# Performance work log

Measured on AMD Instinct MI355X. Metric: run time of the kernel, lower is better.

Reference implementation:

```python
import jax, jax.numpy as jnp
import numpy as np

N_NODES = 10000
N_EDGES = 160000
D_IN = 128
D_EMB = 512
D_HID = 256
GAT_SLOPE = 0.2   # PyG GATv2Conv default negative_slope
MLP_SLOPE = 0.1   # relu_alpha


def _glorot(key, shape):
    fan_in, fan_out = shape[0], shape[-1]
    lim = np.sqrt(6.0 / (fan_in + fan_out))
    return jax.random.uniform(key, shape, jnp.float32, -lim, lim)


def setup_inputs() -> dict:
    key = jax.random.key(0)
    ks = jax.random.split(key, 20)
    inp = {
        'x': jax.random.normal(ks[0], (N_NODES, D_IN), jnp.float32),
        'edge_index': jax.random.randint(ks[1], (2, N_EDGES), 0, N_NODES, jnp.int64),
    }
    # GATv2 layers: (Wl, Wr, att, bias) each
    dims = [(D_IN, D_EMB), (D_EMB, D_EMB), (D_EMB, D_EMB)]
    for i, (di, do) in enumerate(dims, start=1):
        inp[f'Wl{i}'] = _glorot(ks[2 + 4 * i], (di, do))
        inp[f'Wr{i}'] = _glorot(ks[3 + 4 * i], (di, do))
        inp[f'att{i}'] = _glorot(ks[4 + 4 * i], (1, do))[0]
        inp[f'b{i}'] = jnp.zeros((do,), jnp.float32)
    # MLP
    inp['A1'] = _glorot(ks[2], (D_EMB, D_HID)); inp['c1'] = jnp.zeros((D_HID,), jnp.float32)
    inp['A2'] = _glorot(ks[3], (D_HID, D_HID)); inp['c2'] = jnp.zeros((D_HID,), jnp.float32)
    inp['A3'] = _glorot(ks[4], (D_HID, 1));     inp['c3'] = jnp.zeros((1,), jnp.float32)
    return inp


def gatv2_conv(x, src, dst, Wl, Wr, att, bias):
    # PyG GATv2Conv, heads=1: xl = source transform, xr = target transform
    xl = x @ Wl                                   # [N, D]
    xr = x @ Wr                                   # [N, D]
    # per-edge attention logit: att . leaky_relu(xl[src] + xr[dst])
    e = jax.nn.leaky_relu(xl[src] + xr[dst], GAT_SLOPE) @ att   # [E]
    # segment softmax over incoming edges of each dst node
    emax = jax.ops.segment_max(e, dst, num_segments=N_NODES)    # [N]
    w = jnp.exp(e - emax[dst])
    denom = jax.ops.segment_sum(w, dst, num_segments=N_NODES)   # [N]
    alpha = w / (denom[dst] + 1e-16)                             # [E]
    out = jax.ops.segment_sum(alpha[:, None] * xl[src], dst, num_segments=N_NODES)
    return out + bias


def reference(x, edge_index, Wl1, Wr1, att1, b1, Wl2, Wr2, att2, b2,
              Wl3, Wr3, att3, b3, A1, c1, A2, c2, A3, c3):
    src, dst = edge_index[0], edge_index[1]
    h = jnp.tanh(gatv2_conv(x, src, dst, Wl1, Wr1, att1, b1))
    h = jnp.tanh(gatv2_conv(h, src, dst, Wl2, Wr2, att2, b2))
    h = jnp.tanh(gatv2_conv(h, src, dst, Wl3, Wr3, att3, b3))
    h = jax.nn.leaky_relu(h @ A1 + c1, MLP_SLOPE)
    h = jax.nn.leaky_relu(h @ A2 + c2, MLP_SLOPE)
    logits = h @ A3 + c3                          # [N, 1]
    return jax.nn.softmax(logits, axis=0)         # softmax over nodes
```

## Files before the change

### kernel.cpp

```cpp
#include <hip/hip_runtime.h>
#include <hip/hip_bf16.h>

#define N_NODES 10000
#define N_EDGES 160000
#define D_IN    128
#define D_EMB   512
#define D_HID   256
#define DMAX    512

typedef unsigned short u16;
typedef __attribute__((ext_vector_type(8))) short short8;
typedef __attribute__((ext_vector_type(4))) float floatx4;

__device__ __forceinline__ float bf2f(u16 u) {
    union { unsigned int i; float f; } v; v.i = ((unsigned int)u) << 16; return v.f;
}
__device__ __forceinline__ u16 f2bf(float f) {
    union { float f; unsigned int i; } v; v.f = f;
    unsigned int x = v.i;
    return (u16)((x + 0x7fffu + ((x >> 16) & 1u)) >> 16);
}
__device__ __forceinline__ float inval(const void* p, int fp32, int idx) {
    return fp32 ? ((const float*)p)[idx] : bf2f(((const u16*)p)[idx]);
}

__device__ __forceinline__ void gld_lds16(const u16* g, u16* l) {
    __builtin_amdgcn_global_load_lds((const __attribute__((address_space(1))) void*)g,
                                     (__attribute__((address_space(3))) void*)l,
                                     16, 0, 0);
}

__device__ __forceinline__ int edge_src(const int* __restrict__ ei, int flg, int e) {
    int v = flg ? ei[2 * e] : ei[e];
    return min(max(v, 0), N_NODES - 1);
}
__device__ __forceinline__ int edge_dst(const int* __restrict__ ei, int flg, int e) {
    int v = flg ? ei[2 * N_EDGES + 2 * e] : ei[N_EDGES + e];
    return min(max(v, 0), N_NODES - 1);
}

__global__ void sentinel_kernel(float* out, int n) {
    int i = blockIdx.x * 256 + threadIdx.x;
    if (i < n) out[i] = 1.0f;
}

__global__ __launch_bounds__(256)
void detect_zero_kernel(const int* __restrict__ ei, const u16* __restrict__ xu,
                        int* flag, int* counts, float* logits) {
    int gid = blockIdx.x * 256 + threadIdx.x;
    for (int i = gid; i < N_NODES; i += gridDim.x * 256) { counts[i] = 0; logits[i] = 0.f; }
    if (blockIdx.x != 0) return;
    __shared__ int s_or[256];
    __shared__ int s_cnt[256];
    int t = threadIdx.x;
    int v = 0;
    for (int k = t; k < 4096; k += 256) v |= ei[1 + 2 * k];
    int c = 0;
    for (int k = t; k < 4096; k += 256) {
        u16 u = xu[k];
        int ex = (u >> 7) & 0xFF;
        bool plaus = (u == 0) || (ex >= 64 && ex <= 191);
        if (!plaus) c++;
    }
    s_or[t] = v; s_cnt[t] = c;
    __syncthreads();
    for (int off = 128; off > 0; off >>= 1) {
        if (t < off) { s_or[t] |= s_or[t + off]; s_cnt[t] += s_cnt[t + off]; }
        __syncthreads();
    }
    if (t == 0) {
        flag[0] = (s_or[0] == 0) ? 1 : 0;
        flag[1] = (s_cnt[0] > 256) ? 1 : 0;
    }
}

struct ConvJobs {
    const void* src[10];
    u16* dh[10];
    u16* dl[10];
    int rows[10], cols[10], trans[10];
    int cum[11];
    int njobs;
};

__global__ __launch_bounds__(256)
void convert_fused_kernel(ConvJobs jobs, const int* __restrict__ flag) {
    int idx = blockIdx.x * 256 + threadIdx.x;
    if (idx >= jobs.cum[jobs.njobs]) return;
    int fp32 = flag[1];
    int jb = 0;
    while (idx >= jobs.cum[jb + 1]) jb++;
    int local = idx - jobs.cum[jb];
    float v = inval(jobs.src[jb], fp32, local);
    u16 hi = f2bf(v);
    int o;
    if (jobs.trans[jb]) {
        int r = local / jobs.cols[jb], c = local % jobs.cols[jb];
        o = c * jobs.rows[jb] + r;
    } else o = local;
    jobs.dh[jb][o] = hi;
    if (jobs.dl[jb]) jobs.dl[jb][o] = f2bf(v - bf2f(hi));
}

__global__ void count_edges_kernel(const int* __restrict__ ei, const int* __restrict__ flag,
                                   int* counts) {
    int e = blockIdx.x * 256 + threadIdx.x;
    if (e < N_EDGES) atomicAdd(&counts[edge_dst(ei, flag[0], e)], 1);
}

__global__ __launch_bounds__(256)
void scan_counts_kernel(int* counts, int* rowptr) {
    __shared__ int part[256];
    int tid = threadIdx.x;
    const int CH = 40;
    int base = tid * CH;
    int loc[CH];
    int s = 0;
    #pragma unroll
    for (int i = 0; i < CH; i++) {
        int idx = base + i;
        int c = (idx < N_NODES) ? counts[idx] : 0;
        loc[i] = s; s += c;
    }
    part[tid] = s;
    __syncthreads();
    for (int off = 1; off < 256; off <<= 1) {
        int v = part[tid];
        int add = (tid >= off) ? part[tid - off] : 0;
        __syncthreads();
        part[tid] = v + add;
        __syncthreads();
    }
    int pre = (tid > 0) ? part[tid - 1] : 0;
    #pragma unroll
    for (int i = 0; i < CH; i++) {
        int idx = base + i;
        if (idx < N_NODES) { int v = pre + loc[i]; rowptr[idx] = v; counts[idx] = v; }
    }
    if (tid == 255) rowptr[N_NODES] = part[255];
}

__global__ void fill_esrcp_kernel(const int* __restrict__ ei, const int* __restrict__ flag,
                                  int* counts, int* esrcp) {
    int e = blockIdx.x * 256 + threadIdx.x;
    if (e < N_EDGES) {
        int flg = flag[0];
        int pos = atomicAdd(&counts[edge_dst(ei, flg, e)], 1);
        if (pos >= 0 && pos < N_EDGES) esrcp[pos] = edge_src(ei, flg, e);
    }
}

__global__ __launch_bounds__(256)
void lpt_order_kernel(const int* __restrict__ rowptr, int* __restrict__ order) {
    __shared__ int hist[DMAX];
    __shared__ int off[DMAX];
    __shared__ int part[256];
    int t = threadIdx.x;
    for (int d = t; d < DMAX; d += 256) hist[d] = 0;
    __syncthreads();
    for (int n = t; n < N_NODES; n += 256) {
        int d = min(rowptr[n + 1] - rowptr[n], DMAX - 1);
        atomicAdd(&hist[d], 1);
    }
    __syncthreads();
    int d0 = (DMAX - 1) - 2 * t;
    int d1 = d0 - 1;
    int c0 = hist[d0], c1 = hist[d1];
    part[t] = c0 + c1;
    __syncthreads();
    for (int o = 1; o < 256; o <<= 1) {
        int v = part[t];
        int add = (t >= o) ? part[t - o] : 0;
        __syncthreads();
        part[t] = v + add;
        __syncthreads();
    }
    int pre = (t > 0) ? part[t - 1] : 0;
    off[d0] = pre;
    off[d1] = pre + c0;
    __syncthreads();
    for (int n = t; n < N_NODES; n += 256) {
        int d = min(rowptr[n + 1] - rowptr[n], DMAX - 1);
        int pos = atomicAdd(&off[d], 1);
        if (pos >= 0 && pos < N_NODES) order[pos] = n;
    }
}

__global__ __launch_bounds__(256)
void gemm_dual_kernel(const u16* __restrict__ Ah, const u16* __restrict__ Al,
                      const u16* __restrict__ B0h, const u16* __restrict__ B1h,
                      u16* __restrict__ C0, float* __restrict__ C1,
                      int M, int N, int K)
{
    __shared__ u16 sAh[128 * 32];
    __shared__ u16 sAl[128 * 32];
    __shared__ u16 sBh[128 * 32];
    int nb = N >> 7;
    int half = (int)blockIdx.x >= nb;
    int bx = half ? (blockIdx.x - nb) : blockIdx.x;
    const u16* BTh = half ? B1h : B0h;

    int tid = threadIdx.x;
    int lane = tid & 63, wv = tid >> 6;
    int l15 = lane & 15, l4 = lane >> 4;
    int wr = (wv >> 1) * 64, wc = (wv & 1) * 64;
    int m0 = blockIdx.y * 128, n0 = bx * 128;

    int i0 = tid, i1 = tid + 256;
    int r0 = i0 >> 2, b0 = i0 & 3, sb0 = b0 ^ ((r0 >> 1) & 3);
    int r1 = i1 >> 2, b1 = i1 & 3, sb1 = b1 ^ ((r1 >> 1) & 3);
    int gr0 = min(m0 + r0, M - 1), gr1 = min(m0 + r1, M - 1);
    const u16* a0p = Ah + (size_t)gr0 * K + sb0 * 8;
    const u16* a1p = Ah + (size_t)gr1 * K + sb1 * 8;
    const u16* l0p = Al + (size_t)gr0 * K + sb0 * 8;
    const u16* l1p = Al + (size_t)gr1 * K + sb1 * 8;
    const u16* bb0p = BTh + (size_t)(n0 + r0) * K + sb0 * 8;
    const u16* bb1p = BTh + (size_t)(n0 + r1) * K + sb1 * 8;
    u16* lA0 = &sAh[(size_t)(wv * 64) * 8];
    u16* lA1 = &sAh[(size_t)(256 + wv * 64) * 8];
    u16* lL0 = &sAl[(size_t)(wv * 64) * 8];
    u16* lL1 = &sAl[(size_t)(256 + wv * 64) * 8];
    u16* lB0 = &sBh[(size_t)(wv * 64) * 8];
    u16* lB1 = &sBh[(size_t)(256 + wv * 64) * 8];

    floatx4 acc[4][4];
    #pragma unroll
    for (int i = 0; i < 4; i++)
        #pragma unroll
        for (int j = 0; j < 4; j++) acc[i][j] = (floatx4){0.f, 0.f, 0.f, 0.f};

    int aoff[4], boff[4];
    #pragma unroll
    for (int i = 0; i < 4; i++) {
        int arow = wr + i * 16 + l15;
        aoff[i] = arow * 32 + ((l4 ^ ((arow >> 1) & 3)) << 3);
        int bcol = wc + i * 16 + l15;
        boff[i] = bcol * 32 + ((l4 ^ ((bcol >> 1) & 3)) << 3);
    }

    for (int kk = 0; kk < K; kk += 32) {
        __syncthreads();
        gld_lds16(a0p + kk, lA0);
        gld_lds16(a1p + kk, lA1);
        gld_lds16(l0p + kk, lL0);
        gld_lds16(l1p + kk, lL1);
        gld_lds16(bb0p + kk, lB0);
        gld_lds16(bb1p + kk, lB1);
        __syncthreads();

        short8 ah[4], al[4];
        #pragma unroll
        for (int i = 0; i < 4; i++) {
            ah[i] = *(const short8*)(&sAh[aoff[i]]);
            al[i] = *(const short8*)(&sAl[aoff[i]]);
        }
        #pragma unroll
        for (int j = 0; j < 4; j++) {
            short8 bh = *(const short8*)(&sBh[boff[j]]);
            #pragma unroll
            for (int i = 0; i < 4; i++) {
                acc[i][j] = __builtin_amdgcn_mfma_f32_16x16x32_bf16(ah[i], bh, acc[i][j], 0, 0, 0);
                acc[i][j] = __builtin_amdgcn_mfma_f32_16x16x32_bf16(al[i], bh, acc[i][j], 0, 0, 0);
            }
        }
    }

    #pragma unroll
    for (int j = 0; j < 4; j++) {
        int col = n0 + wc + j * 16 + l15;
        #pragma unroll
        for (int i = 0; i < 4; i++) {
            #pragma unroll
            for (int r = 0; r < 4; r++) {
                int row = m0 + wr + i * 16 + l4 * 4 + r;
                if (row < M) {
                    if (half) C1[(size_t)row * N + col] = acc[i][j][r];
                    else      C0[(size_t)row * N + col] = f2bf(acc[i][j][r]);
                }
            }
        }
    }
}

template<int FUSE>
__global__ __launch_bounds__(256)
void gemm_mlp64_kernel(const u16* __restrict__ Ah, const u16* __restrict__ Al,
                       const u16* __restrict__ BTh,
                       u16* __restrict__ Ch, u16* __restrict__ Cl,
                       const void* __restrict__ biasraw,
                       const void* __restrict__ A3raw, float* __restrict__ logits,
                       const int* __restrict__ flag,
                       int M, int N, int K)
{
    __shared__ u16 sAh[64 * 32];
    __shared__ u16 sAl[64 * 32];
    __shared__ u16 sBh[64 * 32];
    int tid = threadIdx.x;
    int lane = tid & 63, wv = tid >> 6;
    int l15 = lane & 15, l4 = lane >> 4;
    int m0 = blockIdx.y * 64, n0 = blockIdx.x * 64;

    int r = (tid >> 2), blk = tid & 3, sb = blk ^ ((r >> 1) & 3);
    int gr = min(m0 + r, M - 1);
    const u16* ap = Ah + (size_t)gr * K + sb * 8;
    const u16* lp = Al + (size_t)gr * K + sb * 8;
    const u16* bp = BTh + (size_t)(n0 + r) * K + sb * 8;
    u16* lA = &sAh[(size_t)(wv * 64) * 8];
    u16* lL = &sAl[(size_t)(wv * 64) * 8];
    u16* lB = &sBh[(size_t)(wv * 64) * 8];

    floatx4 acc[4];
    #pragma unroll
    for (int j = 0; j < 4; j++) acc[j] = (floatx4){0.f, 0.f, 0.f, 0.f};

    int arow = wv * 16 + l15;
    int aoff = arow * 32 + ((l4 ^ ((arow >> 1) & 3)) << 3);
    int boff[4];
    #pragma unroll
    for (int j = 0; j < 4; j++) {
        int bcol = j * 16 + l15;
        boff[j] = bcol * 32 + ((l4 ^ ((bcol >> 1) & 3)) << 3);
    }

    for (int kk = 0; kk < K; kk += 32) {
        __syncthreads();
        gld_lds16(ap + kk, lA);
        gld_lds16(lp + kk, lL);
        gld_lds16(bp + kk, lB);
        __syncthreads();

        short8 ah = *(const short8*)(&sAh[aoff]);
        short8 al = *(const short8*)(&sAl[aoff]);
        #pragma unroll
        for (int j = 0; j < 4; j++) {
            short8 bh = *(const short8*)(&sBh[boff[j]]);
            acc[j] = __builtin_amdgcn_mfma_f32_16x16x32_bf16(ah, bh, acc[j], 0, 0, 0);
            acc[j] = __builtin_amdgcn_mfma_f32_16x16x32_bf16(al, bh, acc[j], 0, 0, 0);
        }
    }

    const int fp32 = flag[1];
    float lsum[4] = {0.f, 0.f, 0.f, 0.f};
    #pragma unroll
    for (int j = 0; j < 4; j++) {
        int col = n0 + j * 16 + l15;
        float bv = inval(biasraw, fp32, col);
        float a3 = FUSE ? inval(A3raw, fp32, col) : 0.f;
        #pragma unroll
        for (int rr = 0; rr < 4; rr++) {
            int row = m0 + wv * 16 + l4 * 4 + rr;
            if (row < M) {
                float v = acc[j][rr] + bv;
                v = v > 0.f ? v : 0.1f * v;
                if (FUSE) {
                    lsum[rr] += v * a3;
                } else {
                    u16 hi = f2bf(v);
                    Ch[(size_t)row * N + col] = hi;
                    Cl[(size_t)row * N + col] = f2bf(v - bf2f(hi));
                }
            }
        }
    }
    if (FUSE) {
        #pragma unroll
        for (int rr = 0; rr < 4; rr++) {
            float s = lsum[rr];
            s += __shfl_xor(s, 1);
            s += __shfl_xor(s, 2);
            s += __shfl_xor(s, 4);
            s += __shfl_xor(s, 8);
            int row = m0 + wv * 16 + l4 * 4 + rr;
            if (l15 == 0 && row < M) atomicAdd(&logits[row], s);
        }
    }
}

__global__ __launch_bounds__(256)
void gat_wave_kernel(const int* __restrict__ rowptr, const int* __restrict__ esrcp,
                     const int* __restrict__ order,
                     const u16* __restrict__ xlb, const float* __restrict__ xr,
                     const void* __restrict__ att, const void* __restrict__ bias,
                     const int* __restrict__ flag,
                     u16* __restrict__ hh, u16* __restrict__ hl)
{
    int lane = threadIdx.x & 63, wv = threadIdx.x >> 6;
    int slot = blockIdx.x * 4 + wv;
    if (slot >= N_NODES) return;
    int n = order[slot];
    n = min(max(n, 0), N_NODES - 1);
    int fp32 = flag[1];
    int d0 = lane * 8;
    int l3 = lane & 3;

    int beg = rowptr[n], end = rowptr[n + 1];
    int deg = end - beg;
    int ng = (deg + 3) >> 2;

    const u16* xbase = xlb + d0;

    const float* xrr = xr + (size_t)n * D_EMB;
    float4 r0 = *(const float4*)(xrr + d0);
    float4 r1 = *(const float4*)(xrr + d0 + 4);
    float xrv[8] = {r0.x, r0.y, r0.z, r0.w, r1.x, r1.y, r1.z, r1.w};
    float attv[8];
    #pragma unroll
    for (int k = 0; k < 8; k++) attv[k] = inval(att, fp32, d0 + k);

    float m_run = -3.4e38f, s_run = 0.f;
    float acc[8] = {0.f, 0.f, 0.f, 0.f, 0.f, 0.f, 0.f, 0.f};

    auto ldidx = [&](int g) -> int {
        return esrcp[min(beg + 4 * g + l3, N_EDGES - 1)];
    };

    if (ng > 0) {
        int i0 = ldidx(0);
        uint4 cu0, cu1, cu2, cu3;
        {
            int s0 = __shfl(i0, 0), s1 = __shfl(i0, 1), s2 = __shfl(i0, 2), s3 = __shfl(i0, 3);
            cu0 = *(const uint4*)(xbase + (size_t)s0 * D_EMB);
            cu1 = *(const uint4*)(xbase + (size_t)s1 * D_EMB);
            cu2 = *(const uint4*)(xbase + (size_t)s2 * D_EMB);
            cu3 = *(const uint4*)(xbase + (size_t)s3 * D_EMB);
        }
        int nidx = (ng > 1) ? ldidx(1) : 0;

        for (int g = 0; g < ng; g++) {
            uint4 nu0, nu1, nu2, nu3;
            int nidx2 = 0;
            bool have_next = (g + 1 < ng);
            if (have_next) {
                int t0 = __shfl(nidx, 0), t1 = __shfl(nidx, 1),
                    t2 = __shfl(nidx, 2), t3 = __shfl(nidx, 3);
                nu0 = *(const uint4*)(xbase + (size_t)t0 * D_EMB);
                nu1 = *(const uint4*)(xbase + (size_t)t1 * D_EMB);
                nu2 = *(const uint4*)(xbase + (size_t)t2 * D_EMB);
                nu3 = *(const uint4*)(xbase + (size_t)t3 * D_EMB);
                if (g + 2 < ng) nidx2 = ldidx(g + 2);
            }

            union { uint4 q; u16 us[8]; } u0, u1, u2, u3;
            u0.q = cu0; u1.q = cu1; u2.q = cu2; u3.q = cu3;
            float v0[8], v1[8], v2[8], v3[8];
            #pragma unroll
            for (int k = 0; k < 8; k++) {
                v0[k] = bf2f(u0.us[k]); v1[k] = bf2f(u1.us[k]);
                v2[k] = bf2f(u2.us[k]); v3[k] = bf2f(u3.us[k]);
            }
            float e0 = 0.f, e1 = 0.f, e2 = 0.f, e3 = 0.f;
            #pragma unroll
            for (int k = 0; k < 8; k++) {
                float t0 = v0[k] + xrv[k]; t0 = fmaxf(t0, 0.2f * t0); e0 += attv[k] * t0;
                float t1 = v1[k] + xrv[k]; t1 = fmaxf(t1, 0.2f * t1); e1 += attv[k] * t1;
                float t2 = v2[k] + xrv[k]; t2 = fmaxf(t2, 0.2f * t2); e2 += attv[k] * t2;
                float t3 = v3[k] + xrv[k]; t3 = fmaxf(t3, 0.2f * t3); e3 += attv[k] * t3;
            }
            #pragma unroll
            for (int o = 32; o > 0; o >>= 1) {
                e0 += __shfl_xor(e0, o);
                e1 += __shfl_xor(e1, o);
                e2 += __shfl_xor(e2, o);
                e3 += __shfl_xor(e3, o);
            }
            int base = beg + 4 * g;
            if (base + 1 >= end) e1 = -3.4e38f;
            if (base + 2 >= end) e2 = -3.4e38f;
            if (base + 3 >= end) e3 = -3.4e38f;
            float m4 = fmaxf(fmaxf(e0, e1), fmaxf(e2, e3));
            float m_new = fmaxf(m_run, m4);
            float sc = __expf(m_run - m_new);
            float w0 = __expf(e0 - m_new), w1 = __expf(e1 - m_new);
            float w2 = __expf(e2 - m_new), w3 = __expf(e3 - m_new);
            s_run = s_run * sc + (w0 + w1) + (w2 + w3);
            #pragma unroll
            for (int k = 0; k < 8; k++)
                acc[k] = acc[k] * sc + w0 * v0[k] + w1 * v1[k] + w2 * v2[k] + w3 * v3[k];
            m_run = m_new;

            if (have_next) {
                cu0 = nu0; cu1 = nu1; cu2 = nu2; cu3 = nu3;
                nidx = nidx2;
            }
        }
    }

    float inv = 1.f / (s_run + 1e-16f);
    union { uint4 q; u16 us[8]; } ph, pl;
    #pragma unroll
    for (int k = 0; k < 8; k++) {
        float h = tanhf(acc[k] * inv + inval(bias, fp32, d0 + k));
        u16 hi = f2bf(h);
        ph.us[k] = hi;
        pl.us[k] = f2bf(h - bf2f(hi));
    }
    *(uint4*)(&hh[(size_t)n * D_EMB + d0]) = ph.q;
    *(uint4*)(&hl[(size_t)n * D_EMB + d0]) = pl.q;
}

__global__ __launch_bounds__(256)
void softmax_kernel(const float* __restrict__ logits, float* __restrict__ out)
{
    __shared__ float red[4];
    __shared__ float s_m, s_s;
    int tid = threadIdx.x, lane = tid & 63, wv = tid >> 6;
    float m = -3.4e38f;
    for (int i = tid; i < N_NODES; i += 256) m = fmaxf(m, logits[i]);
    #pragma unroll
    for (int o = 32; o > 0; o >>= 1) m = fmaxf(m, __shfl_down(m, o));
    if (lane == 0) red[wv] = m;
    __syncthreads();
    if (tid == 0) {
        float mm = red[0];
        for (int i = 1; i < 4; i++) mm = fmaxf(mm, red[i]);
        s_m = mm;
    }
    __syncthreads();
    float mm = s_m;
    float s = 0.f;
    for (int i = tid; i < N_NODES; i += 256) s += __expf(logits[i] - mm);
    #pragma unroll
    for (int o = 32; o > 0; o >>= 1) s += __shfl_down(s, o);
    if (lane == 0) red[wv] = s;
    __syncthreads();
    if (tid == 0) {
        float ss = 0.f;
        for (int i = 0; i < 4; i++) ss += red[i];
        s_s = ss;
    }
    __syncthreads();
    float invs = 1.f / s_s;
    for (int i = tid; i < N_NODES; i += 256) out[i] = __expf(logits[i] - mm) * invs;
}

extern "C" void kernel_launch(void* const* d_in, const int* in_sizes, int n_in,
                              void* d_out, int out_size, void* d_ws, size_t ws_size,
                              hipStream_t stream)
{
    const void* x   = d_in[0];
    const int*  ei  = (const int*)d_in[1];
    const void* Wl[3]  = {d_in[2],  d_in[6],  d_in[10]};
    const void* Wr[3]  = {d_in[3],  d_in[7],  d_in[11]};
    const void* att[3] = {d_in[4],  d_in[8],  d_in[12]};
    const void* bia[3] = {d_in[5],  d_in[9],  d_in[13]};
    const void* A1 = d_in[14];
    const void* c1 = d_in[15];
    const void* A2 = d_in[16];
    const void* c2 = d_in[17];
    const void* A3 = d_in[18];

    char* p = (char*)d_ws;
    auto alloc = [&](size_t bytes) {
        char* r = p;
        p += (bytes + 255) & ~(size_t)255;
        return r;
    };
    u16*   xlb    = (u16*)  alloc((size_t)N_NODES * D_EMB * 4);
    float* xr     = (float*)alloc((size_t)N_NODES * D_EMB * 4);
    u16*   hh     = (u16*)  alloc((size_t)N_NODES * D_EMB * 2);
    u16*   hl     = (u16*)  alloc((size_t)N_NODES * D_EMB * 2);
    int*   esrcp  = (int*)  alloc((size_t)N_EDGES * 4);
    int*   rowptr = (int*)  alloc((size_t)(N_NODES + 1) * 4);
    int*   counts = (int*)  alloc((size_t)N_NODES * 4);
    int*   flag   = (int*)  alloc(256);
    float* logits = (float*)alloc((size_t)N_NODES * 4);
    int*   order  = (int*)  alloc((size_t)N_NODES * 4);
    u16* wl1h = (u16*)alloc(D_EMB * D_IN  * 2);
    u16* wr1h = (u16*)alloc(D_EMB * D_IN  * 2);
    u16* wl2h = (u16*)alloc(D_EMB * D_EMB * 2);
    u16* wr2h = (u16*)alloc(D_EMB * D_EMB * 2);
    u16* wl3h = (u16*)alloc(D_EMB * D_EMB * 2);
    u16* wr3h = (u16*)alloc(D_EMB * D_EMB * 2);
    u16* a1h  = (u16*)alloc(D_EMB * D_HID * 2);
    u16* a2h  = (u16*)alloc(D_HID * D_HID * 2);
    u16* xph  = (u16*)alloc((size_t)N_NODES * D_IN * 2);
    u16* xpl  = (u16*)alloc((size_t)N_NODES * D_IN * 2);
    size_t needed = (size_t)(p - (char*)d_ws);

    if (ws_size < needed) {
        sentinel_kernel<<<(out_size + 255) / 256, 256, 0, stream>>>((float*)d_out, out_size);
        return;
    }

    u16* m1h = (u16*)xlb;
    u16* m1l = (u16*)((char*)xlb + 5120000);

    detect_zero_kernel<<<40, 256, 0, stream>>>(ei, (const u16*)x, flag, counts, logits);
    count_edges_kernel<<<(N_EDGES + 255) / 256, 256, 0, stream>>>(ei, flag, counts);
    scan_counts_kernel<<<1, 256, 0, stream>>>(counts, rowptr);
    fill_esrcp_kernel<<<(N_EDGES + 255) / 256, 256, 0, stream>>>(ei, flag, counts, esrcp);

    lpt_order_kernel<<<1, 256, 0, stream>>>(rowptr, order);

    ConvJobs jobs;
    auto setjob = [&](int i, const void* s, u16* dh, u16* dl, int r, int c, int tr) {
        jobs.src[i] = s; jobs.dh[i] = dh; jobs.dl[i] = dl;
        jobs.rows[i] = r; jobs.cols[i] = c; jobs.trans[i] = tr;
    };
    setjob(0, x,     xph,  xpl,     N_NODES, D_IN, 0);
    setjob(1, Wl[0], wl1h, nullptr, D_IN,  D_EMB, 1);
    setjob(2, Wr[0], wr1h, nullptr, D_IN,  D_EMB, 1);
    setjob(3, Wl[1], wl2h, nullptr, D_EMB, D_EMB, 1);
    setjob(4, Wr[1], wr2h, nullptr, D_EMB, D_EMB, 1);
    setjob(5, Wl[2], wl3h, nullptr, D_EMB, D_EMB, 1);
    setjob(6, Wr[2], wr3h, nullptr, D_EMB, D_EMB, 1);
    setjob(7, A1,    a1h,  nullptr, D_EMB, D_HID, 1);
    setjob(8, A2,    a2h,  nullptr, D_HID, D_HID, 1);
    jobs.njobs = 9;
    jobs.cum[0] = 0;
    for (int i = 0; i < 9; i++) jobs.cum[i + 1] = jobs.cum[i] + jobs.rows[i] * jobs.cols[i];
    int ctotal = jobs.cum[9];
    convert_fused_kernel<<<(ctotal + 255) / 256, 256, 0, stream>>>(jobs, flag);

    dim3 gdual(2 * D_EMB / 128, (N_NODES + 127) / 128);
    dim3 gmlp64(D_HID / 64, (N_NODES + 63) / 64);
    int gatgrid = (N_NODES + 3) / 4;

    gemm_dual_kernel<<<gdual, 256, 0, stream>>>(xph, xpl, wl1h, wr1h, xlb, xr, N_NODES, D_EMB, D_IN);
    gat_wave_kernel<<<gatgrid, 256, 0, stream>>>(rowptr, esrcp, order, xlb, xr, att[0], bia[0], flag, hh, hl);
    gemm_dual_kernel<<<gdual, 256, 0, stream>>>(hh, hl, wl2h, wr2h, xlb, xr, N_NODES, D_EMB, D_EMB);
    gat_wave_kernel<<<gatgrid, 256, 0, stream>>>(rowptr, esrcp, order, xlb, xr, att[1], bia[1], flag, hh, hl);
    gemm_dual_kernel<<<gdual, 256, 0, stream>>>(hh, hl, wl3h, wr3h, xlb, xr, N_NODES, D_EMB, D_EMB);
    gat_wave_kernel<<<gatgrid, 256, 0, stream>>>(rowptr, esrcp, order, xlb, xr, att[2], bia[2], flag, hh, hl);

    gemm_mlp64_kernel<0><<<gmlp64, 256, 0, stream>>>(hh, hl, a1h, m1h, m1l, c1, nullptr, nullptr, flag, N_NODES, D_HID, D_EMB);
    gemm_mlp64_kernel<1><<<gmlp64, 256, 0, stream>>>(m1h, m1l, a2h, nullptr, nullptr, c2, A3, logits, flag, N_NODES, D_HID, D_HID);
    softmax_kernel<<<1, 256, 0, stream>>>(logits, (float*)d_out);
}
```

Measured before the change: 438.9 us.

## Parallelize LPT degree-ordering across blocks with histogram, scan, scatter kernels

```diff
diff --git a/kernel.cpp b/kernel.cpp
--- a/kernel.cpp
+++ b/kernel.cpp
@@ -46,9 +46,10 @@
 
 __global__ __launch_bounds__(256)
 void detect_zero_kernel(const int* __restrict__ ei, const u16* __restrict__ xu,
-                        int* flag, int* counts, float* logits) {
+                        int* flag, int* counts, float* logits, int* ghist) {
     int gid = blockIdx.x * 256 + threadIdx.x;
     for (int i = gid; i < N_NODES; i += gridDim.x * 256) { counts[i] = 0; logits[i] = 0.f; }
+    for (int i = gid; i < DMAX; i += gridDim.x * 256) ghist[i] = 0;
     if (blockIdx.x != 0) return;
     __shared__ int s_or[256];
     __shared__ int s_cnt[256];
@@ -151,21 +152,30 @@
 }
 
 __global__ __launch_bounds__(256)
-void lpt_order_kernel(const int* __restrict__ rowptr, int* __restrict__ order) {
-    __shared__ int hist[DMAX];
-    __shared__ int off[DMAX];
+void lpt_hist_kernel(const int* __restrict__ rowptr, int* __restrict__ ghist) {
+    __shared__ int lhist[DMAX];
+    int t = threadIdx.x;
+    for (int d = t; d < DMAX; d += 256) lhist[d] = 0;
+    __syncthreads();
+    int n = blockIdx.x * 256 + t;
+    if (n < N_NODES) {
+        int d = min(rowptr[n + 1] - rowptr[n], DMAX - 1);
+        atomicAdd(&lhist[d], 1);
+    }
+    __syncthreads();
+    for (int d = t; d < DMAX; d += 256) {
+        int c = lhist[d];
+        if (c > 0) atomicAdd(&ghist[d], c);
+    }
+}
+
+__global__ __launch_bounds__(256)
+void lpt_scan_kernel(const int* __restrict__ ghist, int* __restrict__ doff) {
     __shared__ int part[256];
     int t = threadIdx.x;
-    for (int d = t; d < DMAX; d += 256) hist[d] = 0;
-    __syncthreads();
-    for (int n = t; n < N_NODES; n += 256) {
-        int d = min(rowptr[n + 1] - rowptr[n], DMAX - 1);
-        atomicAdd(&hist[d], 1);
-    }
-    __syncthreads();
     int d0 = (DMAX - 1) - 2 * t;
     int d1 = d0 - 1;
-    int c0 = hist[d0], c1 = hist[d1];
+    int c0 = ghist[d0], c1 = ghist[d1];
     part[t] = c0 + c1;
     __syncthreads();
     for (int o = 1; o < 256; o <<= 1) {
@@ -176,12 +186,34 @@
         __syncthreads();
     }
     int pre = (t > 0) ? part[t - 1] : 0;
-    off[d0] = pre;
-    off[d1] = pre + c0;
-    __syncthreads();
-    for (int n = t; n < N_NODES; n += 256) {
-        int d = min(rowptr[n + 1] - rowptr[n], DMAX - 1);
-        int pos = atomicAdd(&off[d], 1);
+    doff[d0] = pre;
+    doff[d1] = pre + c0;
+}
+
+__global__ __launch_bounds__(256)
+void lpt_scatter_kernel(const int* __restrict__ rowptr, int* __restrict__ doff,
+                        int* __restrict__ order) {
+    __shared__ int lhist[DMAX];
+    __shared__ int lbase[DMAX];
+    int t = threadIdx.x;
+    for (int d = t; d < DMAX; d += 256) lhist[d] = 0;
+    __syncthreads();
+    int n = blockIdx.x * 256 + t;
+    int dg = 0;
+    if (n < N_NODES) {
+        dg = min(rowptr[n + 1] - rowptr[n], DMAX - 1);
+        atomicAdd(&lhist[dg], 1);
+    }
+    __syncthreads();
+    for (int d = t; d < DMAX; d += 256) {
+        int c = lhist[d];
+        lbase[d] = (c > 0) ? atomicAdd(&doff[d], c) : 0;
+        lhist[d] = 0;
+    }
+    __syncthreads();
+    if (n < N_NODES) {
+        int rank = atomicAdd(&lhist[dg], 1);
+        int pos = lbase[dg] + rank;
         if (pos >= 0 && pos < N_NODES) order[pos] = n;
     }
 }
@@ -564,6 +596,8 @@
     int*   counts = (int*)  alloc((size_t)N_NODES * 4);
     int*   flag   = (int*)  alloc(256);
     float* logits = (float*)alloc((size_t)N_NODES * 4);
+    int*   ghist  = (int*)  alloc(DMAX * 4);
+    int*   doff   = (int*)  alloc(DMAX * 4);
     int*   order  = (int*)  alloc((size_t)N_NODES * 4);
     u16* wl1h = (u16*)alloc(D_EMB * D_IN  * 2);
     u16* wr1h = (u16*)alloc(D_EMB * D_IN  * 2);
@@ -585,12 +619,15 @@
     u16* m1h = (u16*)xlb;
     u16* m1l = (u16*)((char*)xlb + 5120000);
 
-    detect_zero_kernel<<<40, 256, 0, stream>>>(ei, (const u16*)x, flag, counts, logits);
+    detect_zero_kernel<<<40, 256, 0, stream>>>(ei, (const u16*)x, flag, counts, logits, ghist);
     count_edges_kernel<<<(N_EDGES + 255) / 256, 256, 0, stream>>>(ei, flag, counts);
     scan_counts_kernel<<<1, 256, 0, stream>>>(counts, rowptr);
     fill_esrcp_kernel<<<(N_EDGES + 255) / 256, 256, 0, stream>>>(ei, flag, counts, esrcp);
 
-    lpt_order_kernel<<<1, 256, 0, stream>>>(rowptr, order);
+    int nblk = (N_NODES + 255) / 256;
+    lpt_hist_kernel<<<nblk, 256, 0, stream>>>(rowptr, ghist);
+    lpt_scan_kernel<<<1, 256, 0, stream>>>(ghist, doff);
+    lpt_scatter_kernel<<<nblk, 256, 0, stream>>>(rowptr, doff, order);
 
     ConvJobs jobs;
     auto setjob = [&](int i, const void* s, u16* dh, u16* dl, int r, int c, int tr) {
```

Result: faster. 425.4 us (-3.1%).
